# Optimization experiments

Hardware: AMD Instinct MI355X
Metric: run time of the kernel (lower is better)

## Reference

```python
import jax, jax.numpy as jnp
import numpy as np

K = 7  # hardcoded pooling grid in the module


def setup_inputs() -> dict:
    key = jax.random.key(0)
    k1, k2, k3, k4, k5 = jax.random.split(key, 5)
    B, C1, H, W = 4, 21, 100, 100
    cls_conv_out = jax.random.normal(k1, (B, C1 * K * K, H, W), dtype=jnp.float32)
    n = 2000
    # ROIs: (ymin, xmin, ymax, xmax) integer coords; spans >= K so bin steps >= 1
    ymin = jax.random.randint(k2, (n,), 0, 40)
    ylen = jax.random.randint(k3, (n,), K, 57)
    xmin = jax.random.randint(k4, (n,), 0, 40)
    xlen = jax.random.randint(k5, (n,), K, 57)
    rois = jnp.stack([ymin, xmin, ymin + ylen, xmin + xlen], axis=1).astype(jnp.int32)
    return {"cls_conv_out": cls_conv_out, "rois": rois}


def _ps_roi_pool(cls_conv_out, rois):
    k = K
    B, C, H, W = cls_conv_out.shape
    c1 = C // (k * k)
    # Original indexes batch element `_ - 1` where `_` is the batch size -> last element.
    # Channel ordering from the `count` counter: channel = (j*k + l)*c1 + cls.
    feat = cls_conv_out[B - 1].reshape(k, k, c1, H, W)
    # Integral image (summed-area table) so each variable-size bin mean is 4 gathers.
    I = jnp.pad(feat, ((0, 0), (0, 0), (0, 0), (1, 0), (1, 0))).cumsum(axis=3).cumsum(axis=4)  # [k,k,c1,H+1,W+1]

    ymin, xmin, ymax, xmax = rois[:, 0], rois[:, 1], rois[:, 2], rois[:, 3]
    ys = (ymax - ymin) // k  # per-ROI bin step (int floor, as in int(range/k))
    xs = (xmax - xmin) // k
    j = jnp.arange(k)
    y0 = ymin[:, None] + j[None, :] * ys[:, None]  # [n,k] bin starts
    y1 = y0 + ys[:, None]                          # [n,k] bin stops
    x0 = xmin[:, None] + j[None, :] * xs[:, None]
    x1 = x0 + xs[:, None]

    jj = j[None, :, None, None]
    ll = j[None, None, :, None]
    cc = jnp.arange(c1)[None, None, None, :]
    Y0 = y0[:, :, None, None]; Y1 = y1[:, :, None, None]
    X0 = x0[:, None, :, None]; X1 = x1[:, None, :, None]
    # bin sums via SAT: [n, k, k, c1]
    S = (I[jj, ll, cc, Y1, X1] - I[jj, ll, cc, Y0, X1]
         - I[jj, ll, cc, Y1, X0] + I[jj, ll, cc,0*Y0 + Y0, X0])
    area = (ys * xs).astype(S.dtype)[:, None, None, None]
    pooled = S / area  # per-bin mean -> pooling_track, layout [n,k,k,c1]
    return pooled


def reference(cls_conv_out, rois):
    pooled = _ps_roi_pool(cls_conv_out, rois)          # [n,k,k,c1]
    avg = pooled.mean(axis=(1, 2))                     # AvgPool2d((7,7)) -> [n,c1]
    # nn.Softmax() on a 4D tensor applies over dim=1 (classes)
    scores = jax.nn.softmax(avg, axis=1)[:, :, None, None]  # [n,c1,1,1]
    return scores
```

## Files before the change

### kernel.cpp

```cpp
#include <hip/hip_runtime.h>
#include <math.h>

#define KK      7
#define C1      21
#define NPLANES (KK * KK * C1)
#define H       100
#define W       100
#define TS      101

__global__ __launch_bounds__(256) void plane_partial(
    const float* __restrict__ src,
    size_t batch_off,
    const int*  __restrict__ rois,
    int nrois,
    float* __restrict__ partial)
{
    const int p  = blockIdx.x;
    const int jl = p / C1;
    const int l  = jl % KK;
    const int j  = jl / KK;
    const int t  = threadIdx.x;

    __shared__ float tile[H * TS];

    {
        const float4* p4 = (const float4*)(src + batch_off + (size_t)p * (H * W));
        for (int i = t; i < (H * W) / 4; i += 256) {
            float4 v = p4[i];
            int g = i * 4;
            int y = g / W, x = g - y * W;
            float* d = &tile[y * TS + x];
            d[0] = v.x; d[1] = v.y; d[2] = v.z; d[3] = v.w;
        }
    }
    __syncthreads();

    if (t < H) {
        float s = 0.f;
        float* row = &tile[t * TS];
        for (int x = 0; x < W; ++x) { s += row[x]; row[x] = s; }
    }
    __syncthreads();

    if (t < W) {
        float s = 0.f;
        for (int y = 0; y < H; ++y) { s += tile[y * TS + t]; tile[y * TS + t] = s; }
    }
    __syncthreads();

    float* prow = partial + (size_t)p * nrois;
    for (int n = t; n < nrois; n += 256) {
        const int4 r  = ((const int4*)rois)[n];
        const int ys  = (r.z - r.x) / KK;
        const int xs  = (r.w - r.y) / KK;
        const int y0  = r.x + j * ys;
        const int x0  = r.y + l * xs;
        const int y1  = y0 + ys - 1;
        const int x1  = x0 + xs - 1;

        float S = tile[y1 * TS + x1];
        if (x0 > 0)           S -= tile[y1 * TS + (x0 - 1)];
        if (y0 > 0)           S -= tile[(y0 - 1) * TS + x1];
        if (y0 > 0 && x0 > 0) S += tile[(y0 - 1) * TS + (x0 - 1)];

        prow[n] = S;
    }
}

#define RB 16

__global__ __launch_bounds__(256) void reduce_softmax(
    const float* __restrict__ partial,
    const int*   __restrict__ rois,
    int nrois,
    float*       __restrict__ out)
{
    const int dn = threadIdx.x & (RB - 1);
    const int cg = threadIdx.x / RB;
    const int n  = blockIdx.x * RB + dn;

    __shared__ float ch[RB][C1];

    if (n < nrois) {
        for (int c = cg; c < C1; c += 16) {
            float s = 0.f;
            const float* pc = partial + (size_t)c * nrois + n;
            #pragma unroll
            for (int jl = 0; jl < KK * KK; ++jl) {
                s += pc[(size_t)jl * C1 * nrois];
            }
            ch[dn][c] = s;
        }
    }
    __syncthreads();

    if (threadIdx.x < RB) {
        const int n2 = blockIdx.x * RB + threadIdx.x;
        if (n2 < nrois) {
            const int4 r  = ((const int4*)rois)[n2];
            const int ys  = (r.z - r.x) / KK;
            const int xs  = (r.w - r.y) / KK;
            const float inv = 1.0f / (49.0f * (float)(ys * xs));

            float v[C1];
            float m = -INFINITY;
            #pragma unroll
            for (int c = 0; c < C1; ++c) {
                v[c] = ch[threadIdx.x][c] * inv;
                m = fmaxf(m, v[c]);
            }
            float s = 0.f;
            #pragma unroll
            for (int c = 0; c < C1; ++c) { v[c] = __expf(v[c] - m); s += v[c]; }
            const float rs = 1.0f / s;
            #pragma unroll
            for (int c = 0; c < C1; ++c) out[(size_t)n2 * C1 + c] = v[c] * rs;
        }
    }
}

__global__ __launch_bounds__(256) void roi_pool_direct(
    const float* __restrict__ src,
    size_t batch_off,
    const int*   __restrict__ rois,
    float*       __restrict__ out)
{
    const int n = blockIdx.x;
    const int t = threadIdx.x;

    __shared__ float chsum[C1];
    if (t < C1) chsum[t] = 0.f;
    __syncthreads();

    const int ymin = rois[4 * n + 0];
    const int xmin = rois[4 * n + 1];
    const int ymax = rois[4 * n + 2];
    const int xmax = rois[4 * n + 3];
    const int ys = (ymax - ymin) / KK;
    const int xs = (xmax - xmin) / KK;

    const float* base = src + batch_off;

    for (int idx = t; idx < NPLANES; idx += blockDim.x) {
        const int c  = idx % C1;
        const int jl = idx / C1;
        const int l  = jl % KK;
        const int j  = jl / KK;
        const int y0 = ymin + j * ys;
        const int x0 = xmin + l * xs;
        const float* plane = base + (size_t)idx * (H * W);
        float s = 0.f;
        for (int y = y0; y < y0 + ys; ++y) {
            const float* row = plane + (size_t)y * W + x0;
            for (int x = 0; x < xs; ++x) s += row[x];
        }
        atomicAdd(&chsum[c], s);
    }
    __syncthreads();

    if (t == 0) {
        const float inv = 1.0f / (49.0f * (float)(ys * xs));
        float m = -INFINITY;
        float v[C1];
        for (int c = 0; c < C1; ++c) { v[c] = chsum[c] * inv; m = fmaxf(m, v[c]); }
        float s = 0.f;
        for (int c = 0; c < C1; ++c) { v[c] = expf(v[c] - m); s += v[c]; }
        const float rs = 1.0f / s;
        for (int c = 0; c < C1; ++c) out[(size_t)n * C1 + c] = v[c] * rs;
    }
}

extern "C" void kernel_launch(void* const* d_in, const int* in_sizes, int n_in,
                              void* d_out, int out_size, void* d_ws, size_t ws_size,
                              hipStream_t stream)
{
    const float* cls  = (const float*)d_in[0];
    const int*   rois = (const int*)d_in[1];
    float*       out  = (float*)d_out;

    const int nrois = in_sizes[1] / 4;
    const size_t plane_elems = (size_t)NPLANES * H * W;
    const int B = (int)((size_t)in_sizes[0] / plane_elems);
    const size_t batch_off = (size_t)(B - 1) * plane_elems;

    const size_t need = (size_t)NPLANES * nrois * sizeof(float);
    if (ws_size >= need) {
        float* partial = (float*)d_ws;
        plane_partial<<<NPLANES, 256, 0, stream>>>(cls, batch_off, rois, nrois, partial);
        reduce_softmax<<<(nrois + RB - 1) / RB, 256, 0, stream>>>(partial, rois, nrois, out);
    } else {
        roi_pool_direct<<<nrois, 256, 0, stream>>>(cls, batch_off, rois, out);
    }
}
```

Before: 218.8 us.

## Process two planes per block with register prefetch of the second plane

Each block of plane_partial now handles two planes. While the first plane's integral image is built and queried, the second plane's data is held in registers (10 float4 per thread), then copied into shared memory. The goal is to hide global load latency behind the scan work. The cost is half as many blocks (515 instead of 1029), which may hurt occupancy on 256 CUs, plus higher register pressure.

```diff
diff --git a/kernel.cpp b/kernel.cpp
--- a/kernel.cpp
+++ b/kernel.cpp
@@ -7,6 +7,8 @@
 #define H       100
 #define W       100
 #define TS      101
+#define NCHUNK  ((H * W) / 4)
+#define PREFK   10
 
 __global__ __launch_bounds__(256) void plane_partial(
     const float* __restrict__ src,
@@ -15,55 +17,92 @@
     int nrois,
     float* __restrict__ partial)
 {
-    const int p  = blockIdx.x;
-    const int jl = p / C1;
-    const int l  = jl % KK;
-    const int j  = jl / KK;
     const int t  = threadIdx.x;
+    const int p0 = blockIdx.x * 2;
+    const int p1 = p0 + 1;
+    const bool has_p1 = (p1 < NPLANES);
 
     __shared__ float tile[H * TS];
 
     {
-        const float4* p4 = (const float4*)(src + batch_off + (size_t)p * (H * W));
-        for (int i = t; i < (H * W) / 4; i += 256) {
-            float4 v = p4[i];
-            int g = i * 4;
-            int y = g / W, x = g - y * W;
-            float* d = &tile[y * TS + x];
-            d[0] = v.x; d[1] = v.y; d[2] = v.z; d[3] = v.w;
-        }
-    }
-    __syncthreads();
-
-    if (t < H) {
-        float s = 0.f;
-        float* row = &tile[t * TS];
-        for (int x = 0; x < W; ++x) { s += row[x]; row[x] = s; }
-    }
-    __syncthreads();
-
-    if (t < W) {
-        float s = 0.f;
-        for (int y = 0; y < H; ++y) { s += tile[y * TS + t]; tile[y * TS + t] = s; }
-    }
-    __syncthreads();
-
-    float* prow = partial + (size_t)p * nrois;
-    for (int n = t; n < nrois; n += 256) {
-        const int4 r  = ((const int4*)rois)[n];
-        const int ys  = (r.z - r.x) / KK;
-        const int xs  = (r.w - r.y) / KK;
-        const int y0  = r.x + j * ys;
-        const int x0  = r.y + l * xs;
-        const int y1  = y0 + ys - 1;
-        const int x1  = x0 + xs - 1;
-
-        float S = tile[y1 * TS + x1];
-        if (x0 > 0)           S -= tile[y1 * TS + (x0 - 1)];
-        if (y0 > 0)           S -= tile[(y0 - 1) * TS + x1];
-        if (y0 > 0 && x0 > 0) S += tile[(y0 - 1) * TS + (x0 - 1)];
-
-        prow[n] = S;
+        const float4* p4 = (const float4*)(src + batch_off + (size_t)p0 * (H * W));
+        #pragma unroll
+        for (int k = 0; k < PREFK; ++k) {
+            int i = t + 256 * k;
+            if (i < NCHUNK) {
+                float4 v = p4[i];
+                int g = i * 4;
+                int y = g / W, x = g - y * W;
+                float* d = &tile[y * TS + x];
+                d[0] = v.x; d[1] = v.y; d[2] = v.z; d[3] = v.w;
+            }
+        }
+    }
+    __syncthreads();
+
+    float4 pref[PREFK];
+    if (has_p1) {
+        const float4* p4 = (const float4*)(src + batch_off + (size_t)p1 * (H * W));
+        #pragma unroll
+        for (int k = 0; k < PREFK; ++k) {
+            int i = t + 256 * k;
+            if (i < NCHUNK) pref[k] = p4[i];
+        }
+    }
+
+    for (int pass = 0; pass < 2; ++pass) {
+        const int p = p0 + pass;
+        if (p >= NPLANES) break;
+        const int jl = p / C1;
+        const int l  = jl % KK;
+        const int j  = jl / KK;
+
+        if (pass == 1) {
+            __syncthreads();
+            #pragma unroll
+            for (int k = 0; k < PREFK; ++k) {
+                int i = t + 256 * k;
+                if (i < NCHUNK) {
+                    float4 v = pref[k];
+                    int g = i * 4;
+                    int y = g / W, x = g - y * W;
+                    float* d = &tile[y * TS + x];
+                    d[0] = v.x; d[1] = v.y; d[2] = v.z; d[3] = v.w;
+                }
+            }
+            __syncthreads();
+        }
+
+        if (t < H) {
+            float s = 0.f;
+            float* row = &tile[t * TS];
+            for (int x = 0; x < W; ++x) { s += row[x]; row[x] = s; }
+        }
+        __syncthreads();
+
+        if (t < W) {
+            float s = 0.f;
+            for (int y = 0; y < H; ++y) { s += tile[y * TS + t]; tile[y * TS + t] = s; }
+        }
+        __syncthreads();
+
+        float* prow = partial + (size_t)p * nrois;
+        for (int n = t; n < nrois; n += 256) {
+            const int4 r  = ((const int4*)rois)[n];
+            const int ys  = (r.z - r.x) / KK;
+            const int xs  = (r.w - r.y) / KK;
+            const int y0  = r.x + j * ys;
+            const int x0  = r.y + l * xs;
+            const int y1  = y0 + ys - 1;
+            const int x1  = x0 + xs - 1;
+
+            float S = tile[y1 * TS + x1];
+            if (x0 > 0)           S -= tile[y1 * TS + (x0 - 1)];
+            if (y0 > 0)           S -= tile[(y0 - 1) * TS + x1];
+            if (y0 > 0 && x0 > 0) S += tile[(y0 - 1) * TS + (x0 - 1)];
+
+            prow[n] = S;
+        }
     }
 }
 
@@ -186,7 +225,8 @@
     const size_t need = (size_t)NPLANES * nrois * sizeof(float);
     if (ws_size >= need) {
         float* partial = (float*)d_ws;
-        plane_partial<<<NPLANES, 256, 0, stream>>>(cls, batch_off, rois, nrois, partial);
+        const int nblocks = (NPLANES + 1) / 2;
+        plane_partial<<<nblocks, 256, 0, stream>>>(cls, batch_off, rois, nrois, partial);
         reduce_softmax<<<(nrois + RB - 1) / RB, 256, 0, stream>>>(partial, rois, nrois, out);
     } else {
         roi_pool_direct<<<nrois, 256, 0, stream>>>(cls, batch_off, rois, out);
```

New measurement: 216.4 us. No clear change (-1.1%).
